# Kernel tuning notes

Hardware: AMD Instinct MI355X
Metric: run time of the kernel (lower is better)

## Reference

```python
import jax, jax.numpy as jnp
import numpy as np

N, S, Q, P = 100000, 64, 50, 3  # pauli words, heads, qubits, pauli basis
EPS = 1e-12  # F.normalize clamp


def setup_inputs() -> dict:
    key = jax.random.key(0)
    k1, k2, k3, k4 = jax.random.split(key, 4)
    return {
        "batch_pauli_tensor": jax.random.uniform(k1, (N, Q, P), dtype=jnp.float32),
        "batch_coeff": jax.random.normal(k2, (N,), dtype=jnp.float32),
        "heads_param": jax.random.normal(k3, (S, Q, P), dtype=jnp.float32),
        "head_ratios_param": jax.random.normal(k4, (S,), dtype=jnp.float32),
    }


def reference(batch_pauli_tensor, batch_coeff, heads_param, head_ratios_param):
    s = heads_param.shape[0]
    heads = jax.nn.softplus(heads_param * 20.0)
    heads = heads / jnp.maximum(jnp.sum(heads, axis=-1, keepdims=True), EPS)
    hr = jax.nn.softplus(head_ratios_param * 20.0)
    hr = hr / jnp.maximum(jnp.sum(hr), EPS)
    hr = (hr + 0.001 / s) / 1.001
    # coverage: per-(word, head, qubit) match prob -> product over qubits -> ratio-weighted sum
    cov = jnp.einsum('nqp,sqp->nsq', batch_pauli_tensor, heads)  # [n, s, q]
    cov = jnp.prod(cov, axis=-1)                                 # [n, s]
    cov = jnp.einsum('s,ns->n', hr, cov)                         # [n]
    # variance loss
    return jnp.sum(batch_coeff ** 2 / cov)
```

## Files before the change

### kernel.cpp

```cpp
#include <hip/hip_runtime.h>
#include <math.h>

#define N_Q 50
#define N_P 3
#define N_S 64
#define ROW 150
#define BLK_ROWS 128
#define THREADS 512
#define WAVES 8
#define SCHUNK 8

#define WS_CNT_OFF 6272
#define WS_HP_OFF 6336
#define WS_HRV_OFF 44736

__device__ __forceinline__ float softplus20(float x) {
    float z = x * 20.0f;
    return fmaxf(z, 0.0f) + log1pf(expf(-fabsf(z)));
}

__global__ void precompute_kernel(const float* __restrict__ heads_param,
                                  const float* __restrict__ hr_param,
                                  float* __restrict__ HP,
                                  float* __restrict__ hrv,
                                  int* __restrict__ cnt) {
    const int tid = threadIdx.x;
    if (blockIdx.x == 0) {
        if (tid == 0) *cnt = 0;
        if (tid < N_S) {
            float sp = softplus20(hr_param[tid]);
            float tot = sp;
            #pragma unroll
            for (int off = 32; off; off >>= 1) tot += __shfl_xor(tot, off);
            float hr = sp / fmaxf(tot, 1e-12f);
            hrv[tid] = (hr + 0.001f / (float)N_S) / 1.001f;
        }
    }
    int idx = blockIdx.x * blockDim.x + tid;
    if (idx < N_S * N_Q) {
        int q = idx / N_S;
        int s = idx - q * N_S;
        const float* hp = heads_param + ((size_t)s * N_Q + q) * N_P;
        float sp0 = softplus20(hp[0]);
        float sp1 = softplus20(hp[1]);
        float sp2 = softplus20(hp[2]);
        float denom = fmaxf(sp0 + sp1 + sp2, 1e-12f);
        float* o = HP + ((size_t)q * N_S + s) * 3;
        o[0] = sp0 / denom;
        o[1] = sp1 / denom;
        o[2] = sp2 / denom;
    }
}

__device__ __forceinline__ void computeQ2(const float4* __restrict__ Hq,
                                          float a0, float a1, float a2,
                                          float c0, float c1, float c2,
                                          float (&p)[SCHUNK], float (&p2)[SCHUNK]) {
    #pragma unroll
    for (int g = 0; g < SCHUNK / 4; ++g) {
        float4 b0 = Hq[3 * g], b1 = Hq[3 * g + 1], b2 = Hq[3 * g + 2];
        p [4*g+0] *= fmaf(b0.x, a0, fmaf(b0.y, a1, b0.z * a2));
        p2[4*g+0] *= fmaf(b0.x, c0, fmaf(b0.y, c1, b0.z * c2));
        p [4*g+1] *= fmaf(b0.w, a0, fmaf(b1.x, a1, b1.y * a2));
        p2[4*g+1] *= fmaf(b0.w, c0, fmaf(b1.x, c1, b1.y * c2));
        p [4*g+2] *= fmaf(b1.z, a0, fmaf(b1.w, a1, b2.x * a2));
        p2[4*g+2] *= fmaf(b1.z, c0, fmaf(b1.w, c1, b2.x * c2));
        p [4*g+3] *= fmaf(b2.y, a0, fmaf(b2.z, a1, b2.w * a2));
        p2[4*g+3] *= fmaf(b2.y, c0, fmaf(b2.z, c1, b2.w * c2));
    }
}

__global__ __launch_bounds__(THREADS) void main_kernel(
    const float* __restrict__ A, const float* __restrict__ coeff,
    const float* __restrict__ HP, const float* __restrict__ hrv,
    double* __restrict__ partials, int* __restrict__ cnt,
    float* __restrict__ out, int N) {
    __shared__ float hHs[N_Q * N_S * 3];
    __shared__ float hrvl[N_S];
    __shared__ float covs[WAVES][BLK_ROWS];
    __shared__ double redd[2];
    __shared__ double redf[WAVES];
    __shared__ int isLast;

    const int tid = threadIdx.x;
    const int lane = tid & 63;
    const int wave = tid >> 6;
    const int nbase = blockIdx.x * BLK_ROWS;

    for (int i = tid; i < (N_Q * N_S * 3) / 4; i += THREADS)
        ((float4*)hHs)[i] = ((const float4*)HP)[i];
    if (tid < N_S) hrvl[tid] = hrv[tid];
    __syncthreads();

    int n0 = nbase + lane;        if (n0 >= N) n0 = N - 1;
    int n1 = nbase + 64 + lane;   if (n1 >= N) n1 = N - 1;
    const float2* __restrict__ pA0 = (const float2*)A + (size_t)n0 * (ROW / 2);
    const float2* __restrict__ pA1 = (const float2*)A + (size_t)n1 * (ROW / 2);

    float prod0[SCHUNK], prod1[SCHUNK];
    #pragma unroll
    for (int i = 0; i < SCHUNK; ++i) { prod0[i] = 1.0f; prod1[i] = 1.0f; }

    const float4* __restrict__ Hbase = (const float4*)hHs + 6 * wave;

    float2 x0 = pA0[0], x1 = pA0[1], x2 = pA0[2];
    float2 y0 = pA1[0], y1 = pA1[1], y2 = pA1[2];

    #pragma unroll 5
    for (int w = 0; w < N_Q / 2; ++w) {
        const int nb = (w < N_Q / 2 - 1) ? 3 * w + 3 : 0;
        float2 nx0 = pA0[nb], nx1 = pA0[nb + 1], nx2 = pA0[nb + 2];
        float2 ny0 = pA1[nb], ny1 = pA1[nb + 1], ny2 = pA1[nb + 2];
        const float4* Hq = Hbase + 96 * w;
        computeQ2(Hq,      x0.x, x0.y, x1.x,  y0.x, y0.y, y1.x, prod0, prod1);
        computeQ2(Hq + 48, x1.y, x2.x, x2.y,  y1.y, y2.x, y2.y, prod0, prod1);
        x0 = nx0; x1 = nx1; x2 = nx2; y0 = ny0; y1 = ny1; y2 = ny2;
    }

    float acc0 = 0.0f, acc1 = 0.0f;
    const int s0 = wave * SCHUNK;
    #pragma unroll
    for (int i = 0; i < SCHUNK; ++i) {
        float wgt = hrvl[s0 + i];
        acc0 = fmaf(wgt, prod0[i], acc0);
        acc1 = fmaf(wgt, prod1[i], acc1);
    }
    covs[wave][lane] = acc0;
    covs[wave][64 + lane] = acc1;
    __syncthreads();

    if (wave < 2) {
        const int row = wave * 64 + lane;
        const int n = nbase + row;
        float cov = 0.0f;
        #pragma unroll
        for (int wv = 0; wv < WAVES; ++wv) cov += covs[wv][row];
        float term = 0.0f;
        if (n < N) { float c = coeff[n]; term = (c * c) / cov; }
        double td = (double)term;
        #pragma unroll
        for (int off = 32; off; off >>= 1) td += __shfl_down(td, off);
        if (lane == 0) redd[wave] = td;
    }
    __syncthreads();

    if (tid == 0) {
        partials[blockIdx.x] = redd[0] + redd[1];
        __threadfence();
        int v = atomicAdd(cnt, 1);
        isLast = (v == (int)gridDim.x - 1);
    }
    __syncthreads();

    if (isLast) {
        __threadfence();
        double s = 0.0;
        for (int i = tid; i < (int)gridDim.x; i += THREADS) s += partials[i];
        #pragma unroll
        for (int off = 32; off; off >>= 1) s += __shfl_down(s, off);
        if (lane == 0) redf[wave] = s;
        __syncthreads();
        if (tid == 0) {
            double t = 0.0;
            #pragma unroll
            for (int wv = 0; wv < WAVES; ++wv) t += redf[wv];
            out[0] = (float)t;
        }
    }
}

extern "C" void kernel_launch(void* const* d_in, const int* in_sizes, int n_in,
                              void* d_out, int out_size, void* d_ws, size_t ws_size,
                              hipStream_t stream) {
    const float* A           = (const float*)d_in[0];
    const float* coeff       = (const float*)d_in[1];
    const float* heads_param = (const float*)d_in[2];
    const float* hr_param    = (const float*)d_in[3];
    const int N = in_sizes[1];
    const int nblocks = (N + BLK_ROWS - 1) / BLK_ROWS;

    char* ws = (char*)d_ws;
    double* partials = (double*)ws;
    int*   cnt = (int*)(ws + WS_CNT_OFF);
    float* HP  = (float*)(ws + WS_HP_OFF);
    float* hrv = (float*)(ws + WS_HRV_OFF);
    float* out = (float*)d_out;

    const int pre_blocks = (N_S * N_Q + THREADS - 1) / THREADS;
    precompute_kernel<<<pre_blocks, THREADS, 0, stream>>>(heads_param, hr_param,
                                                          HP, hrv, cnt);
    main_kernel<<<nblocks, THREADS, 0, stream>>>(A, coeff, HP, hrv, partials,
                                                 cnt, out, N);
}
```

Measured before the change: 175.1 us.

## Stage input rows in LDS and read head weights from global memory

Each block now copies its 128 input rows into a padded shared-memory tile with a coalesced cooperative load. Previously each lane read its own row directly from global memory with a strided pattern. The head-weight table and ratio weights are no longer staged in LDS and are read from global memory through the cache instead. The tile is reused for the per-wave coverage partials, and the launch bounds now request 4 blocks per CU. The risk is extra global or cache traffic for the weights, which used to be broadcast reads from LDS, plus bank conflicts on the 151-stride tile reads.

```diff
diff --git a/kernel.cpp b/kernel.cpp
--- a/kernel.cpp
+++ b/kernel.cpp
@@ -9,6 +9,7 @@
 #define THREADS 512
 #define WAVES 8
 #define SCHUNK 8
+#define ASTRIDE 151
 
 #define WS_CNT_OFF 6272
 #define WS_HP_OFF 6336
@@ -70,14 +71,12 @@
     }
 }
 
-__global__ __launch_bounds__(THREADS) void main_kernel(
+__global__ __launch_bounds__(THREADS, 4) void main_kernel(
     const float* __restrict__ A, const float* __restrict__ coeff,
     const float* __restrict__ HP, const float* __restrict__ hrv,
     double* __restrict__ partials, int* __restrict__ cnt,
     float* __restrict__ out, int N) {
-    __shared__ float hHs[N_Q * N_S * 3];
-    __shared__ float hrvl[N_S];
-    __shared__ float covs[WAVES][BLK_ROWS];
+    __shared__ float Atile[BLK_ROWS * ASTRIDE];
     __shared__ double redd[2];
     __shared__ double redf[WAVES];
     __shared__ int isLast;
@@ -87,46 +86,53 @@
     const int wave = tid >> 6;
     const int nbase = blockIdx.x * BLK_ROWS;
 
-    for (int i = tid; i < (N_Q * N_S * 3) / 4; i += THREADS)
-        ((float4*)hHs)[i] = ((const float4*)HP)[i];
-    if (tid < N_S) hrvl[tid] = hrv[tid];
-    __syncthreads();
-
-    int n0 = nbase + lane;        if (n0 >= N) n0 = N - 1;
-    int n1 = nbase + 64 + lane;   if (n1 >= N) n1 = N - 1;
-    const float2* __restrict__ pA0 = (const float2*)A + (size_t)n0 * (ROW / 2);
-    const float2* __restrict__ pA1 = (const float2*)A + (size_t)n1 * (ROW / 2);
+    {
+        const float2* __restrict__ Asrc = (const float2*)A;
+        for (int g = tid; g < BLK_ROWS * (ROW / 2); g += THREADS) {
+            int r = g / (ROW / 2);
+            int j = g - r * (ROW / 2);
+            int src = nbase + r; if (src >= N) src = N - 1;
+            float2 v = Asrc[(size_t)src * (ROW / 2) + j];
+            Atile[r * ASTRIDE + 2 * j]     = v.x;
+            Atile[r * ASTRIDE + 2 * j + 1] = v.y;
+        }
+    }
+    __syncthreads();
+
+    const float* __restrict__ Ar0 = Atile + lane * ASTRIDE;
+    const float* __restrict__ Ar1 = Atile + (lane + 64) * ASTRIDE;
 
     float prod0[SCHUNK], prod1[SCHUNK];
     #pragma unroll
     for (int i = 0; i < SCHUNK; ++i) { prod0[i] = 1.0f; prod1[i] = 1.0f; }
 
-    const float4* __restrict__ Hbase = (const float4*)hHs + 6 * wave;
-
-    float2 x0 = pA0[0], x1 = pA0[1], x2 = pA0[2];
-    float2 y0 = pA1[0], y1 = pA1[1], y2 = pA1[2];
+    const float4* __restrict__ Hbase = (const float4*)HP + 6 * wave;
 
     #pragma unroll 5
     for (int w = 0; w < N_Q / 2; ++w) {
-        const int nb = (w < N_Q / 2 - 1) ? 3 * w + 3 : 0;
-        float2 nx0 = pA0[nb], nx1 = pA0[nb + 1], nx2 = pA0[nb + 2];
-        float2 ny0 = pA1[nb], ny1 = pA1[nb + 1], ny2 = pA1[nb + 2];
+        const int o = 6 * w;
+        float a0 = Ar0[o], a1 = Ar0[o+1], a2 = Ar0[o+2];
+        float a3 = Ar0[o+3], a4 = Ar0[o+4], a5 = Ar0[o+5];
+        float c0 = Ar1[o], c1 = Ar1[o+1], c2 = Ar1[o+2];
+        float c3 = Ar1[o+3], c4 = Ar1[o+4], c5 = Ar1[o+5];
         const float4* Hq = Hbase + 96 * w;
-        computeQ2(Hq,      x0.x, x0.y, x1.x,  y0.x, y0.y, y1.x, prod0, prod1);
-        computeQ2(Hq + 48, x1.y, x2.x, x2.y,  y1.y, y2.x, y2.y, prod0, prod1);
-        x0 = nx0; x1 = nx1; x2 = nx2; y0 = ny0; y1 = ny1; y2 = ny2;
+        computeQ2(Hq,      a0, a1, a2,  c0, c1, c2, prod0, prod1);
+        computeQ2(Hq + 48, a3, a4, a5,  c3, c4, c5, prod0, prod1);
     }
 
     float acc0 = 0.0f, acc1 = 0.0f;
-    const int s0 = wave * SCHUNK;
+    const float* __restrict__ hw = hrv + wave * SCHUNK;
     #pragma unroll
     for (int i = 0; i < SCHUNK; ++i) {
-        float wgt = hrvl[s0 + i];
+        float wgt = hw[i];
         acc0 = fmaf(wgt, prod0[i], acc0);
         acc1 = fmaf(wgt, prod1[i], acc1);
     }
-    covs[wave][lane] = acc0;
-    covs[wave][64 + lane] = acc1;
+
+    __syncthreads();
+    float* __restrict__ covs = Atile;
+    covs[wave * BLK_ROWS + lane]      = acc0;
+    covs[wave * BLK_ROWS + 64 + lane] = acc1;
     __syncthreads();
 
     if (wave < 2) {
@@ -134,7 +140,7 @@
         const int n = nbase + row;
         float cov = 0.0f;
         #pragma unroll
-        for (int wv = 0; wv < WAVES; ++wv) cov += covs[wv][row];
+        for (int wv = 0; wv < WAVES; ++wv) cov += covs[wv * BLK_ROWS + row];
         float term = 0.0f;
         if (n < N) { float c = coeff[n]; term = (c * c) / cov; }
         double td = (double)term;
```

New measurement: 182.9 us. 1.04x slower.

## Use persistent blocks that stage A tiles through LDS with register prefetch

Applied to the files above, without the earlier changes.

The main kernel now runs as a fixed grid of 256 persistent blocks, each walking a contiguous range of 128-row tiles. Each tile is loaded with coalesced float2 reads into a padded LDS buffer, replacing the old strided per-lane row reads. The next tile is prefetched into registers while the current one is computed, then written to LDS. This trades extra LDS (about 77KB per block) and register pressure for coalesced global traffic and load/compute overlap, and it also cuts the number of partials to reduce.

```diff
diff --git a/kernel.cpp b/kernel.cpp
--- a/kernel.cpp
+++ b/kernel.cpp
@@ -5,14 +5,19 @@
 #define N_P 3
 #define N_S 64
 #define ROW 150
-#define BLK_ROWS 128
+#define TROWS 128
 #define THREADS 512
 #define WAVES 8
 #define SCHUNK 8
-
-#define WS_CNT_OFF 6272
-#define WS_HP_OFF 6336
-#define WS_HRV_OFF 44736
+#define GRID 256
+#define ASTRIDE 151
+#define NF2 75
+#define TF2 (TROWS * NF2)
+#define NLD 19
+
+#define WS_CNT_OFF 3200
+#define WS_HP_OFF 3264
+#define WS_HRV_OFF 41664
 
 __device__ __forceinline__ float softplus20(float x) {
     float z = x * 20.0f;
@@ -70,14 +75,15 @@
     }
 }
 
-__global__ __launch_bounds__(THREADS) void main_kernel(
+__global__ __launch_bounds__(THREADS, 2) void main_kernel(
     const float* __restrict__ A, const float* __restrict__ coeff,
     const float* __restrict__ HP, const float* __restrict__ hrv,
     double* __restrict__ partials, int* __restrict__ cnt,
     float* __restrict__ out, int N) {
     __shared__ float hHs[N_Q * N_S * 3];
+    __shared__ float Abuf[TROWS * ASTRIDE];
     __shared__ float hrvl[N_S];
-    __shared__ float covs[WAVES][BLK_ROWS];
+    __shared__ float covs[WAVES][TROWS];
     __shared__ double redd[2];
     __shared__ double redf[WAVES];
     __shared__ int isLast;
@@ -85,67 +91,125 @@
     const int tid = threadIdx.x;
     const int lane = tid & 63;
     const int wave = tid >> 6;
-    const int nbase = blockIdx.x * BLK_ROWS;
+
+    const int ntiles = (N + TROWS - 1) / TROWS;
+    const int qn = ntiles / GRID, rn = ntiles % GRID;
+    const int b = blockIdx.x;
+    const int t0 = b * qn + (b < rn ? b : rn);
+    const int tcnt = qn + (b < rn ? 1 : 0);
 
     for (int i = tid; i < (N_Q * N_S * 3) / 4; i += THREADS)
         ((float4*)hHs)[i] = ((const float4*)HP)[i];
     if (tid < N_S) hrvl[tid] = hrv[tid];
+
+    const float2* __restrict__ Ag = (const float2*)A;
+    const size_t A2MAX = (size_t)N * NF2 - 1;
+    float2 st[NLD];
+
+    {
+        const size_t base = (size_t)t0 * TF2;
+        #pragma unroll
+        for (int k = 0; k < NLD; ++k) {
+            int idx = tid + (k << 9);
+            if (idx < TF2) {
+                size_t g = base + idx; if (g > A2MAX) g = A2MAX;
+                st[k] = Ag[g];
+            }
+        }
+        #pragma unroll
+        for (int k = 0; k < NLD; ++k) {
+            int idx = tid + (k << 9);
+            if (idx < TF2) {
+                int r = idx / NF2, c2 = idx - r * NF2;
+                float* d = Abuf + r * ASTRIDE + 2 * c2;
+                d[0] = st[k].x; d[1] = st[k].y;
+            }
+        }
+    }
     __syncthreads();
 
-    int n0 = nbase + lane;        if (n0 >= N) n0 = N - 1;
-    int n1 = nbase + 64 + lane;   if (n1 >= N) n1 = N - 1;
-    const float2* __restrict__ pA0 = (const float2*)A + (size_t)n0 * (ROW / 2);
-    const float2* __restrict__ pA1 = (const float2*)A + (size_t)n1 * (ROW / 2);
-
-    float prod0[SCHUNK], prod1[SCHUNK];
-    #pragma unroll
-    for (int i = 0; i < SCHUNK; ++i) { prod0[i] = 1.0f; prod1[i] = 1.0f; }
-
+    const float* __restrict__ Ar0 = Abuf + lane * ASTRIDE;
+    const float* __restrict__ Ar1 = Abuf + (lane + 64) * ASTRIDE;
     const float4* __restrict__ Hbase = (const float4*)hHs + 6 * wave;
 
-    float2 x0 = pA0[0], x1 = pA0[1], x2 = pA0[2];
-    float2 y0 = pA1[0], y1 = pA1[1], y2 = pA1[2];
-
-    #pragma unroll 5
-    for (int w = 0; w < N_Q / 2; ++w) {
-        const int nb = (w < N_Q / 2 - 1) ? 3 * w + 3 : 0;
-        float2 nx0 = pA0[nb], nx1 = pA0[nb + 1], nx2 = pA0[nb + 2];
-        float2 ny0 = pA1[nb], ny1 = pA1[nb + 1], ny2 = pA1[nb + 2];
-        const float4* Hq = Hbase + 96 * w;
-        computeQ2(Hq,      x0.x, x0.y, x1.x,  y0.x, y0.y, y1.x, prod0, prod1);
-        computeQ2(Hq + 48, x1.y, x2.x, x2.y,  y1.y, y2.x, y2.y, prod0, prod1);
-        x0 = nx0; x1 = nx1; x2 = nx2; y0 = ny0; y1 = ny1; y2 = ny2;
-    }
-
-    float acc0 = 0.0f, acc1 = 0.0f;
-    const int s0 = wave * SCHUNK;
-    #pragma unroll
-    for (int i = 0; i < SCHUNK; ++i) {
-        float wgt = hrvl[s0 + i];
-        acc0 = fmaf(wgt, prod0[i], acc0);
-        acc1 = fmaf(wgt, prod1[i], acc1);
-    }
-    covs[wave][lane] = acc0;
-    covs[wave][64 + lane] = acc1;
-    __syncthreads();
-
-    if (wave < 2) {
-        const int row = wave * 64 + lane;
-        const int n = nbase + row;
-        float cov = 0.0f;
-        #pragma unroll
-        for (int wv = 0; wv < WAVES; ++wv) cov += covs[wv][row];
-        float term = 0.0f;
-        if (n < N) { float c = coeff[n]; term = (c * c) / cov; }
-        double td = (double)term;
-        #pragma unroll
-        for (int off = 32; off; off >>= 1) td += __shfl_down(td, off);
-        if (lane == 0) redd[wave] = td;
-    }
-    __syncthreads();
+    double bsum = 0.0;
+
+    for (int ti = 0; ti < tcnt; ++ti) {
+        const int t = t0 + ti;
+        const bool have = (ti + 1 < tcnt);
+
+        if (have) {
+            const size_t base = (size_t)(t + 1) * TF2;
+            #pragma unroll
+            for (int k = 0; k < NLD; ++k) {
+                int idx = tid + (k << 9);
+                if (idx < TF2) {
+                    size_t g = base + idx; if (g > A2MAX) g = A2MAX;
+                    st[k] = Ag[g];
+                }
+            }
+        }
+
+        float prod0[SCHUNK], prod1[SCHUNK];
+        #pragma unroll
+        for (int i = 0; i < SCHUNK; ++i) { prod0[i] = 1.0f; prod1[i] = 1.0f; }
+
+        #pragma unroll 5
+        for (int w = 0; w < N_Q / 2; ++w) {
+            const int o = 6 * w;
+            float a0 = Ar0[o], a1 = Ar0[o+1], a2 = Ar0[o+2];
+            float a3 = Ar0[o+3], a4 = Ar0[o+4], a5 = Ar0[o+5];
+            float c0 = Ar1[o], c1 = Ar1[o+1], c2 = Ar1[o+2];
+            float c3 = Ar1[o+3], c4 = Ar1[o+4], c5 = Ar1[o+5];
+            const float4* Hq = Hbase + 96 * w;
+            computeQ2(Hq,      a0, a1, a2,  c0, c1, c2, prod0, prod1);
+            computeQ2(Hq + 48, a3, a4, a5,  c3, c4, c5, prod0, prod1);
+        }
+
+        float acc0 = 0.0f, acc1 = 0.0f;
+        const int s0 = wave * SCHUNK;
+        #pragma unroll
+        for (int i = 0; i < SCHUNK; ++i) {
+            float wgt = hrvl[s0 + i];
+            acc0 = fmaf(wgt, prod0[i], acc0);
+            acc1 = fmaf(wgt, prod1[i], acc1);
+        }
+        covs[wave][lane] = acc0;
+        covs[wave][64 + lane] = acc1;
+        __syncthreads();
+
+        if (wave < 2) {
+            const int row = wave * 64 + lane;
+            const int n = t * TROWS + row;
+            float cov = 0.0f;
+            #pragma unroll
+            for (int wv = 0; wv < WAVES; ++wv) cov += covs[wv][row];
+            float term = 0.0f;
+            if (n < N) { float c = coeff[n]; term = (c * c) / cov; }
+            double td = (double)term;
+            #pragma unroll
+            for (int off = 32; off; off >>= 1) td += __shfl_down(td, off);
+            if (lane == 0) redd[wave] = td;
+        }
+
+        if (have) {
+            #pragma unroll
+            for (int k = 0; k < NLD; ++k) {
+                int idx = tid + (k << 9);
+                if (idx < TF2) {
+                    int r = idx / NF2, c2 = idx - r * NF2;
+                    float* d = Abuf + r * ASTRIDE + 2 * c2;
+                    d[0] = st[k].x; d[1] = st[k].y;
+                }
+            }
+        }
+        __syncthreads();
+
+        if (tid == 0) bsum += redd[0] + redd[1];
+    }
 
     if (tid == 0) {
-        partials[blockIdx.x] = redd[0] + redd[1];
+        partials[b] = bsum;
         __threadfence();
         int v = atomicAdd(cnt, 1);
         isLast = (v == (int)gridDim.x - 1);
@@ -161,10 +225,10 @@
         if (lane == 0) redf[wave] = s;
         __syncthreads();
         if (tid == 0) {
-            double t = 0.0;
-            #pragma unroll
-            for (int wv = 0; wv < WAVES; ++wv) t += redf[wv];
-            out[0] = (float)t;
+            double tsum = 0.0;
+            #pragma unroll
+            for (int wv = 0; wv < WAVES; ++wv) tsum += redf[wv];
+            out[0] = (float)tsum;
         }
     }
 }
@@ -177,7 +241,6 @@
     const float* heads_param = (const float*)d_in[2];
     const float* hr_param    = (const float*)d_in[3];
     const int N = in_sizes[1];
-    const int nblocks = (N + BLK_ROWS - 1) / BLK_ROWS;
 
     char* ws = (char*)d_ws;
     double* partials = (double*)ws;
@@ -186,9 +249,9 @@
     float* hrv = (float*)(ws + WS_HRV_OFF);
     float* out = (float*)d_out;
 
-    const int pre_blocks = (N_S * N_Q + THREADS - 1) / THREADS;
-    precompute_kernel<<<pre_blocks, THREADS, 0, stream>>>(heads_param, hr_param,
-                                                          HP, hrv, cnt);
-    main_kernel<<<nblocks, THREADS, 0, stream>>>(A, coeff, HP, hrv, partials,
-                                                 cnt, out, N);
-}
+    const int pre_blocks = (N_S * N_Q + 255) / 256;
+    precompute_kernel<<<pre_blocks, 256, 0, stream>>>(heads_param, hr_param,
+                                                      HP, hrv, cnt);
+    main_kernel<<<GRID, THREADS, 0, stream>>>(A, coeff, HP, hrv, partials,
+                                              cnt, out, N);
+}
```

New measurement: 161.7 us. 7.7% less time.
